# Performance work log

Measured on AMD Instinct MI355X. Metric: run time of the kernel, lower is better.

## Reference

```python
import jax, jax.numpy as jnp
import numpy as np

EMBED_DIM = 1024
NUM_HEADS = 16
HEAD_DIM = EMBED_DIM // NUM_HEADS
LN_EPS = 1e-5


def setup_inputs() -> dict:
    key = jax.random.key(0)
    ks = jax.random.split(key, 6)
    b, s, d = 2, 2048, EMBED_DIM
    scale = 1.0 / np.sqrt(d)
    x = jax.random.normal(ks[0], (b, s, d), dtype=jnp.float32)
    w_qkv = jax.random.normal(ks[1], (d, 3 * d), dtype=jnp.float32) * scale
    b_qkv = jax.random.normal(ks[2], (3 * d,), dtype=jnp.float32) * 0.02
    w_out = jax.random.normal(ks[3], (d, d), dtype=jnp.float32) * scale
    b_out = jax.random.normal(ks[4], (d,), dtype=jnp.float32) * 0.02
    gamma = jnp.ones((d,), dtype=jnp.float32)
    ln_beta = jnp.zeros((d,), dtype=jnp.float32)
    beta = jax.random.normal(ks[5], (), dtype=jnp.float32) * 0.1
    return {"x": x, "w_qkv": w_qkv, "b_qkv": b_qkv, "w_out": w_out,
            "b_out": b_out, "gamma": gamma, "ln_beta": ln_beta, "beta": beta}


def _layernorm(x, gamma, ln_beta):
    mu = jnp.mean(x, axis=-1, keepdims=True)
    var = jnp.mean(jnp.square(x - mu), axis=-1, keepdims=True)
    return (x - mu) * jax.lax.rsqrt(var + LN_EPS) * gamma + ln_beta


def reference(x, w_qkv, b_qkv, w_out, b_out, gamma, ln_beta, beta):
    b, s, d = x.shape
    h, hd = NUM_HEADS, HEAD_DIM
    residual = x
    xn = _layernorm(x, gamma, ln_beta)
    qkv = xn @ w_qkv + b_qkv                       # [b, s, 3d]
    qkv = qkv.reshape(b, s, 3, h, hd)
    q = jnp.transpose(qkv[:, :, 0], (0, 2, 1, 3))  # [b, h, s, hd]
    k = jnp.transpose(qkv[:, :, 1], (0, 2, 1, 3))
    v = jnp.transpose(qkv[:, :, 2], (0, 2, 1, 3))
    attn = jnp.einsum('bhqd,bhkd->bhqk', q, k) / np.sqrt(hd)
    idx = jnp.arange(s)
    dist = jnp.abs(idx[None, :] - idx[:, None]).astype(attn.dtype)  # [s, s]
    attn = attn + beta * jnp.log1p(dist)[None, None, :, :]
    probs = jax.nn.softmax(attn, axis=-1)
    ctx = jnp.einsum('bhqk,bhkd->bhqd', probs, v)  # [b, h, s, hd]
    ctx = jnp.transpose(ctx, (0, 2, 1, 3)).reshape(b, s, d)
    return residual + ctx @ w_out + b_out
```

## Files before the change

### kernel.cpp

```cpp
#include <hip/hip_runtime.h>

#define SEQ 2048
#define DIM 1024
#define NHEAD 16
#define HDIM 64
#define NTOK 4096
#define N3D 3072

typedef __attribute__((ext_vector_type(8))) short bf16x8;
typedef __attribute__((ext_vector_type(4))) float floatx4;
typedef __attribute__((ext_vector_type(4))) unsigned short ushortx4;

__device__ __forceinline__ unsigned short f2bf(float f) {
    unsigned int u = __builtin_bit_cast(unsigned int, f);
    u += 0x7FFFu + ((u >> 16) & 1u);
    return (unsigned short)(u >> 16);
}

__device__ __forceinline__ void async_copy16(const void* g, const void* l) {
    __builtin_amdgcn_global_load_lds(
        (const __attribute__((address_space(1))) unsigned int*)(unsigned long long)g,
        (__attribute__((address_space(3))) unsigned int*)(unsigned int)(unsigned long long)l,
        16, 0, 0);
}

#define MFMA_BF16(a, b, c) __builtin_amdgcn_mfma_f32_16x16x32_bf16((a), (b), (c), 0, 0, 0)

__global__ __launch_bounds__(256)
void transpose_cvt(const float* __restrict__ src, unsigned short* __restrict__ dst,
                   int rows, int cols) {
    __shared__ float tile[32][33];
    const int c0 = blockIdx.x * 32, r0 = blockIdx.y * 32;
    const int tx = threadIdx.x & 31, ty = threadIdx.x >> 5;
    for (int i = 0; i < 4; ++i) {
        int r = ty + i * 8;
        tile[r][tx] = src[(size_t)(r0 + r) * cols + c0 + tx];
    }
    __syncthreads();
    for (int i = 0; i < 4; ++i) {
        int rr = ty + i * 8;
        dst[(size_t)(c0 + rr) * rows + r0 + tx] = f2bf(tile[tx][rr]);
    }
}

__global__ __launch_bounds__(256)
void ln_kernel(const float* __restrict__ x, const float* __restrict__ gamma,
               const float* __restrict__ lnb, unsigned short* __restrict__ xn) {
    const int row = blockIdx.x;
    const int tid = threadIdx.x;
    const float* xr = x + (size_t)row * DIM;
    float4 v = ((const float4*)xr)[tid];
    float s = v.x + v.y + v.z + v.w;
    float s2 = v.x * v.x + v.y * v.y + v.z * v.z + v.w * v.w;
    for (int off = 1; off < 64; off <<= 1) {
        s += __shfl_xor(s, off, 64);
        s2 += __shfl_xor(s2, off, 64);
    }
    __shared__ float red[8];
    const int wave = tid >> 6, lane = tid & 63;
    if (lane == 0) { red[wave] = s; red[4 + wave] = s2; }
    __syncthreads();
    s = red[0] + red[1] + red[2] + red[3];
    s2 = red[4] + red[5] + red[6] + red[7];
    const float mu = s * (1.0f / DIM);
    const float var = s2 * (1.0f / DIM) - mu * mu;
    const float rstd = rsqrtf(var + 1e-5f);
    float4 g = ((const float4*)gamma)[tid];
    float4 bb = ((const float4*)lnb)[tid];
    unsigned short* o = xn + (size_t)row * DIM + tid * 4;
    o[0] = f2bf((v.x - mu) * rstd * g.x + bb.x);
    o[1] = f2bf((v.y - mu) * rstd * g.y + bb.y);
    o[2] = f2bf((v.z - mu) * rstd * g.z + bb.z);
    o[3] = f2bf((v.w - mu) * rstd * g.w + bb.w);
}

__global__ __launch_bounds__(256)
void qkv_gemm(const unsigned short* __restrict__ A, const unsigned short* __restrict__ Bt,
              const float* __restrict__ bias, unsigned short* __restrict__ qo,
              unsigned short* __restrict__ ko, unsigned short* __restrict__ vTo) {
    __shared__ unsigned short Asm[128 * 64];
    __shared__ unsigned short Bsm[128 * 64];
    const int tid = threadIdx.x;
    const int wave = tid >> 6, lane = tid & 63;
    const int quad = lane >> 4, r16 = lane & 15;
    const int m0 = blockIdx.y * 128, n0 = blockIdx.x * 128;
    const int wm = (wave & 1) * 64, wn = (wave >> 1) * 64;
    floatx4 acc[4][4] = {};
    for (int k0 = 0; k0 < DIM; k0 += 64) {
        __syncthreads();
        for (int p = 0; p < 4; ++p) {
            int s = tid + p * 256;
            int r = s >> 3, c8 = (s & 7) << 3;
            async_copy16(A + (size_t)(m0 + r) * DIM + k0 + c8, Asm + s * 8);
            async_copy16(Bt + (size_t)(n0 + r) * DIM + k0 + c8, Bsm + s * 8);
        }
        __syncthreads();
        for (int h = 0; h < 2; ++h) {
            bf16x8 af[4], bfr[4];
            for (int i = 0; i < 4; ++i)
                af[i] = *(const bf16x8*)(Asm + (wm + i * 16 + r16) * 64 + h * 32 + quad * 8);
            for (int j = 0; j < 4; ++j)
                bfr[j] = *(const bf16x8*)(Bsm + (wn + j * 16 + r16) * 64 + h * 32 + quad * 8);
            for (int i = 0; i < 4; ++i)
                for (int j = 0; j < 4; ++j)
                    acc[i][j] = MFMA_BF16(af[i], bfr[j], acc[i][j]);
        }
    }
    for (int j = 0; j < 4; ++j) {
        int n = n0 + wn + j * 16 + r16;
        float bn = bias[n];
        int part = n >> 10, nn = n & 1023;
        int head = nn >> 6, hdi = nn & 63;
        for (int i = 0; i < 4; ++i) {
            int mbase = m0 + wm + i * 16 + quad * 4;
            int bIdx = mbase >> 11, sIdx = mbase & 2047;
            if (part == 2) {
                ushortx4 pack;
                for (int e = 0; e < 4; ++e) pack[e] = f2bf(acc[i][j][e] + bn);
                *(ushortx4*)(vTo + ((size_t)(bIdx * NHEAD + head) * HDIM + hdi) * SEQ + sIdx) = pack;
            } else {
                unsigned short* dst = (part == 0) ? qo : ko;
                for (int e = 0; e < 4; ++e)
                    dst[((size_t)(bIdx * NHEAD + head) * SEQ + sIdx + e) * HDIM + hdi] =
                        f2bf(acc[i][j][e] + bn);
            }
        }
    }
}

__global__ __launch_bounds__(512)
void attn_kernel(const unsigned short* __restrict__ qg, const unsigned short* __restrict__ kg,
                 const unsigned short* __restrict__ vTg, const float* __restrict__ betap,
                 unsigned short* __restrict__ ctx) {
    __shared__ unsigned short QP[128][72];
    __shared__ unsigned short Kd[2][64 * 64];
    __shared__ unsigned short Vd[2][64 * 64];
    __shared__ float logt[SEQ];

    const int tid = threadIdx.x;
    const int wave = tid >> 6, lane = tid & 63;
    const int quad = lane >> 4, r16 = lane & 15;
    const int bh = blockIdx.y, qt = blockIdx.x;
    const int qBase = qt * 128;
    const float betaV = betap[0];
    const float L2E = 1.44269504f;
    const float c1 = 0.125f * L2E;

    for (int i = tid; i < SEQ; i += 512)
        logt[i] = betaV * log1pf((float)i) * L2E - 20.0f;

    const unsigned short* qptr = qg + ((size_t)bh * SEQ + qBase) * HDIM;
    for (int s = tid; s < 1024; s += 512) {
        int r = s >> 3, c8 = (s & 7) << 3;
        *(bf16x8*)(&QP[r][c8]) = *(const bf16x8*)(qptr + r * HDIM + c8);
    }

    const int sr = tid >> 3;
    const int scg = (tid & 7) ^ (sr & 7);
    const unsigned short* kbh = kg + (size_t)bh * SEQ * HDIM;
    const unsigned short* vbh = vTg + (size_t)bh * HDIM * SEQ;
    async_copy16(kbh + (size_t)sr * HDIM + scg * 8, &Kd[0][tid * 8]);
    async_copy16(vbh + (size_t)sr * SEQ + scg * 8, &Vd[0][tid * 8]);
    __syncthreads();

    bf16x8 qf0 = *(const bf16x8*)(&QP[wave * 16 + r16][quad * 8]);
    bf16x8 qf1 = *(const bf16x8*)(&QP[wave * 16 + r16][32 + quad * 8]);

    const bf16x8 onesv = {0x3F80, 0x3F80, 0x3F80, 0x3F80, 0x3F80, 0x3F80, 0x3F80, 0x3F80};

    floatx4 o[5] = {};
    const int qWaveBase = qBase + wave * 16;
    const int qrow0 = qWaveBase + quad * 4;

    for (int kt0 = 0; kt0 < SEQ; kt0 += 64) {
        const int buf = (kt0 >> 6) & 1;
        if (kt0 + 64 < SEQ) {
            async_copy16(kbh + (size_t)(kt0 + 64 + sr) * HDIM + scg * 8, &Kd[buf ^ 1][tid * 8]);
            async_copy16(vbh + (size_t)sr * SEQ + kt0 + 64 + scg * 8, &Vd[buf ^ 1][tid * 8]);
        }

        floatx4 sc[4];
        for (int ct = 0; ct < 4; ++ct) {
            int rK = ct * 16 + r16;
            const unsigned short* kb = &Kd[buf][rK * 64];
            bf16x8 kf0 = *(const bf16x8*)(kb + ((quad ^ (rK & 7)) << 3));
            bf16x8 kf1 = *(const bf16x8*)(kb + (((quad ^ 4) ^ (rK & 7)) << 3));
            floatx4 z = {0.f, 0.f, 0.f, 0.f};
            z = MFMA_BF16(qf0, kf0, z);
            z = MFMA_BF16(qf1, kf1, z);
            sc[ct] = z;
        }
        for (int ct = 0; ct < 4; ++ct) {
            const int keyTile = kt0 + ct * 16;
            const int key = keyTile + r16;
            if (qWaveBase >= keyTile + 16) {
                const float* lp = &logt[qrow0 - key];
                for (int i = 0; i < 4; ++i)
                    sc[ct][i] = __builtin_amdgcn_exp2f(sc[ct][i] * c1 + lp[i]);
            } else if (keyTile >= qWaveBase + 16) {
                const float* lp = &logt[key - qrow0 - 3];
                for (int i = 0; i < 4; ++i)
                    sc[ct][i] = __builtin_amdgcn_exp2f(sc[ct][i] * c1 + lp[3 - i]);
            } else {
                for (int i = 0; i < 4; ++i) {
                    int dist = qrow0 + i - key;
                    dist = dist < 0 ? -dist : dist;
                    sc[ct][i] = __builtin_amdgcn_exp2f(sc[ct][i] * c1 + logt[dist]);
                }
            }
        }
        for (int ct = 0; ct < 4; ++ct)
            for (int i = 0; i < 4; ++i)
                QP[wave * 16 + quad * 4 + i][ct * 16 + r16] = f2bf(sc[ct][i]);
        bf16x8 pf0 = *(const bf16x8*)(&QP[wave * 16 + r16][quad * 8]);
        bf16x8 pf1 = *(const bf16x8*)(&QP[wave * 16 + r16][32 + quad * 8]);
        for (int nt = 0; nt < 4; ++nt) {
            int rV = nt * 16 + r16;
            const unsigned short* vb = &Vd[buf][rV * 64];
            bf16x8 vf0 = *(const bf16x8*)(vb + ((quad ^ (rV & 7)) << 3));
            bf16x8 vf1 = *(const bf16x8*)(vb + (((quad ^ 4) ^ (rV & 7)) << 3));
            o[nt] = MFMA_BF16(pf0, vf0, o[nt]);
            o[nt] = MFMA_BF16(pf1, vf1, o[nt]);
        }
        o[4] = MFMA_BF16(pf0, onesv, o[4]);
        o[4] = MFMA_BF16(pf1, onesv, o[4]);

        __syncthreads();
    }

    const int b_ = bh >> 4, h_ = bh & 15;
    for (int i = 0; i < 4; ++i) {
        float inv = 1.0f / o[4][i];
        int qi = qBase + wave * 16 + quad * 4 + i;
        for (int nt = 0; nt < 4; ++nt) {
            int d = nt * 16 + r16;
            ctx[((size_t)(b_ * SEQ + qi)) * DIM + h_ * HDIM + d] = f2bf(o[nt][i] * inv);
        }
    }
}

__global__ __launch_bounds__(256)
void out_gemm(const unsigned short* __restrict__ A, const unsigned short* __restrict__ Bt,
              const float* __restrict__ bias, const float* __restrict__ resid,
              float* __restrict__ out) {
    __shared__ unsigned short Asm[128 * 64];
    __shared__ unsigned short Bsm[64 * 64];
    const int tid = threadIdx.x;
    const int wave = tid >> 6, lane = tid & 63;
    const int quad = lane >> 4, r16 = lane & 15;
    const int m0 = blockIdx.y * 128, n0 = blockIdx.x * 64;
    const int wm = (wave & 1) * 64, wn = (wave >> 1) * 32;
    floatx4 acc[4][2] = {};
    for (int k0 = 0; k0 < DIM; k0 += 64) {
        __syncthreads();
        for (int p = 0; p < 4; ++p) {
            int s = tid + p * 256;
            int r = s >> 3, c8 = (s & 7) << 3;
            async_copy16(A + (size_t)(m0 + r) * DIM + k0 + c8, Asm + s * 8);
        }
        for (int p = 0; p < 2; ++p) {
            int s = tid + p * 256;
            int r = s >> 3, c8 = (s & 7) << 3;
            async_copy16(Bt + (size_t)(n0 + r) * DIM + k0 + c8, Bsm + s * 8);
        }
        __syncthreads();
        for (int h = 0; h < 2; ++h) {
            bf16x8 af[4], bfr[2];
            for (int i = 0; i < 4; ++i)
                af[i] = *(const bf16x8*)(Asm + (wm + i * 16 + r16) * 64 + h * 32 + quad * 8);
            for (int j = 0; j < 2; ++j)
                bfr[j] = *(const bf16x8*)(Bsm + (wn + j * 16 + r16) * 64 + h * 32 + quad * 8);
            for (int i = 0; i < 4; ++i)
                for (int j = 0; j < 2; ++j)
                    acc[i][j] = MFMA_BF16(af[i], bfr[j], acc[i][j]);
        }
    }
    for (int i = 0; i < 4; ++i)
        for (int j = 0; j < 2; ++j)
            for (int e = 0; e < 4; ++e) {
                int m = m0 + wm + i * 16 + quad * 4 + e;
                int n = n0 + wn + j * 16 + r16;
                out[(size_t)m * DIM + n] = acc[i][j][e] + bias[n] + resid[(size_t)m * DIM + n];
            }
}

extern "C" void kernel_launch(void* const* d_in, const int* in_sizes, int n_in,
                              void* d_out, int out_size, void* d_ws, size_t ws_size,
                              hipStream_t stream) {
    const float* x     = (const float*)d_in[0];
    const float* w_qkv = (const float*)d_in[1];
    const float* b_qkv = (const float*)d_in[2];
    const float* w_out = (const float*)d_in[3];
    const float* b_out = (const float*)d_in[4];
    const float* gamma = (const float*)d_in[5];
    const float* ln_b  = (const float*)d_in[6];
    const float* beta  = (const float*)d_in[7];
    float* out = (float*)d_out;

    char* ws = (char*)d_ws;
    const size_t MB = 1u << 20;
    unsigned short* xn    = (unsigned short*)(ws);
    unsigned short* wqkvT = (unsigned short*)(ws + 8 * MB);
    unsigned short* woutT = (unsigned short*)(ws + 14 * MB);
    unsigned short* qb    = (unsigned short*)(ws + 16 * MB);
    unsigned short* kb    = (unsigned short*)(ws + 24 * MB);
    unsigned short* vTb   = (unsigned short*)(ws + 32 * MB);
    unsigned short* ctx   = xn;

    transpose_cvt<<<dim3(96, 32), 256, 0, stream>>>(w_qkv, wqkvT, DIM, N3D);
    transpose_cvt<<<dim3(32, 32), 256, 0, stream>>>(w_out, woutT, DIM, DIM);
    ln_kernel<<<NTOK, 256, 0, stream>>>(x, gamma, ln_b, xn);
    qkv_gemm<<<dim3(24, 32), 256, 0, stream>>>(xn, wqkvT, b_qkv, qb, kb, vTb);
    attn_kernel<<<dim3(SEQ / 128, 32), 512, 0, stream>>>(qb, kb, vTb, beta, ctx);
    out_gemm<<<dim3(16, 32), 256, 0, stream>>>(ctx, woutT, b_out, x, out);
}
```

Before: 233.1 us.

## Merge prep kernels, swizzle block order for XCDs, add MFMA setprio

The two weight-transpose launches and the layernorm launch become one prep kernel that dispatches on block index, which removes two kernel launches. The qkv GEMM, attention and output GEMM kernels remap their flat block index so that blocks sharing operands land on the same XCD (stride-8 swizzle), aiming for better L2 reuse. The attention kernel raises wave priority around its MFMA sections with s_setprio. The remapping assumes the grid size divides evenly by 8, and the priority hints may interact unpredictably with the wave scheduler.

After: 235.3 us. No clear change (+1.0%).

```diff
diff --git a/kernel.cpp b/kernel.cpp
--- a/kernel.cpp
+++ b/kernel.cpp
@@ -27,51 +27,55 @@
 #define MFMA_BF16(a, b, c) __builtin_amdgcn_mfma_f32_16x16x32_bf16((a), (b), (c), 0, 0, 0)
 
 __global__ __launch_bounds__(256)
-void transpose_cvt(const float* __restrict__ src, unsigned short* __restrict__ dst,
-                   int rows, int cols) {
-    __shared__ float tile[32][33];
-    const int c0 = blockIdx.x * 32, r0 = blockIdx.y * 32;
-    const int tx = threadIdx.x & 31, ty = threadIdx.x >> 5;
-    for (int i = 0; i < 4; ++i) {
-        int r = ty + i * 8;
-        tile[r][tx] = src[(size_t)(r0 + r) * cols + c0 + tx];
-    }
-    __syncthreads();
-    for (int i = 0; i < 4; ++i) {
-        int rr = ty + i * 8;
-        dst[(size_t)(c0 + rr) * rows + r0 + tx] = f2bf(tile[tx][rr]);
-    }
-}
-
-__global__ __launch_bounds__(256)
-void ln_kernel(const float* __restrict__ x, const float* __restrict__ gamma,
-               const float* __restrict__ lnb, unsigned short* __restrict__ xn) {
-    const int row = blockIdx.x;
+void prep_kernel(const float* __restrict__ w_qkv, unsigned short* __restrict__ wqkvT,
+                 const float* __restrict__ w_out, unsigned short* __restrict__ woutT,
+                 const float* __restrict__ x, const float* __restrict__ gamma,
+                 const float* __restrict__ lnb, unsigned short* __restrict__ xn) {
+    const int bid = blockIdx.x;
     const int tid = threadIdx.x;
-    const float* xr = x + (size_t)row * DIM;
-    float4 v = ((const float4*)xr)[tid];
-    float s = v.x + v.y + v.z + v.w;
-    float s2 = v.x * v.x + v.y * v.y + v.z * v.z + v.w * v.w;
-    for (int off = 1; off < 64; off <<= 1) {
-        s += __shfl_xor(s, off, 64);
-        s2 += __shfl_xor(s2, off, 64);
-    }
-    __shared__ float red[8];
-    const int wave = tid >> 6, lane = tid & 63;
-    if (lane == 0) { red[wave] = s; red[4 + wave] = s2; }
-    __syncthreads();
-    s = red[0] + red[1] + red[2] + red[3];
-    s2 = red[4] + red[5] + red[6] + red[7];
-    const float mu = s * (1.0f / DIM);
-    const float var = s2 * (1.0f / DIM) - mu * mu;
-    const float rstd = rsqrtf(var + 1e-5f);
-    float4 g = ((const float4*)gamma)[tid];
-    float4 bb = ((const float4*)lnb)[tid];
-    unsigned short* o = xn + (size_t)row * DIM + tid * 4;
-    o[0] = f2bf((v.x - mu) * rstd * g.x + bb.x);
-    o[1] = f2bf((v.y - mu) * rstd * g.y + bb.y);
-    o[2] = f2bf((v.z - mu) * rstd * g.z + bb.z);
-    o[3] = f2bf((v.w - mu) * rstd * g.w + bb.w);
+    if (bid < 4096) {
+        __shared__ float tile[32][33];
+        const float* src; unsigned short* dst; int cols, bx, by;
+        if (bid < 3072) { src = w_qkv; dst = wqkvT; cols = N3D; bx = bid % 96; by = bid / 96; }
+        else { int t = bid - 3072; src = w_out; dst = woutT; cols = DIM; bx = t & 31; by = t >> 5; }
+        const int c0 = bx * 32, r0 = by * 32;
+        const int tx = tid & 31, ty = tid >> 5;
+        for (int i = 0; i < 4; ++i) {
+            int r = ty + i * 8;
+            tile[r][tx] = src[(size_t)(r0 + r) * cols + c0 + tx];
+        }
+        __syncthreads();
+        for (int i = 0; i < 4; ++i) {
+            int rr = ty + i * 8;
+            dst[(size_t)(c0 + rr) * DIM + r0 + tx] = f2bf(tile[tx][rr]);
+        }
+    } else {
+        const int row = bid - 4096;
+        const float* xr = x + (size_t)row * DIM;
+        float4 v = ((const float4*)xr)[tid];
+        float s = v.x + v.y + v.z + v.w;
+        float s2 = v.x * v.x + v.y * v.y + v.z * v.z + v.w * v.w;
+        for (int off = 1; off < 64; off <<= 1) {
+            s += __shfl_xor(s, off, 64);
+            s2 += __shfl_xor(s2, off, 64);
+        }
+        __shared__ float red[8];
+        const int wave = tid >> 6, lane = tid & 63;
+        if (lane == 0) { red[wave] = s; red[4 + wave] = s2; }
+        __syncthreads();
+        s = red[0] + red[1] + red[2] + red[3];
+        s2 = red[4] + red[5] + red[6] + red[7];
+        const float mu = s * (1.0f / DIM);
+        const float var = s2 * (1.0f / DIM) - mu * mu;
+        const float rstd = rsqrtf(var + 1e-5f);
+        float4 g = ((const float4*)gamma)[tid];
+        float4 bb = ((const float4*)lnb)[tid];
+        unsigned short* o = xn + (size_t)row * DIM + tid * 4;
+        o[0] = f2bf((v.x - mu) * rstd * g.x + bb.x);
+        o[1] = f2bf((v.y - mu) * rstd * g.y + bb.y);
+        o[2] = f2bf((v.z - mu) * rstd * g.z + bb.z);
+        o[3] = f2bf((v.w - mu) * rstd * g.w + bb.w);
+    }
 }
 
 __global__ __launch_bounds__(256)
@@ -83,7 +87,9 @@
     const int tid = threadIdx.x;
     const int wave = tid >> 6, lane = tid & 63;
     const int quad = lane >> 4, r16 = lane & 15;
-    const int m0 = blockIdx.y * 128, n0 = blockIdx.x * 128;
+    const int flat = blockIdx.y * 24 + blockIdx.x;
+    const int swz = (flat & 7) * 96 + (flat >> 3);
+    const int m0 = (swz / 24) * 128, n0 = (swz % 24) * 128;
     const int wm = (wave & 1) * 64, wn = (wave >> 1) * 64;
     floatx4 acc[4][4] = {};
     for (int k0 = 0; k0 < DIM; k0 += 64) {
@@ -140,7 +146,9 @@
     const int tid = threadIdx.x;
     const int wave = tid >> 6, lane = tid & 63;
     const int quad = lane >> 4, r16 = lane & 15;
-    const int bh = blockIdx.y, qt = blockIdx.x;
+    const int flat = blockIdx.y * 16 + blockIdx.x;
+    const int swz = (flat & 7) * 64 + (flat >> 3);
+    const int bh = swz >> 4, qt = swz & 15;
     const int qBase = qt * 128;
     const float betaV = betap[0];
     const float L2E = 1.44269504f;
@@ -180,6 +188,7 @@
         }
 
         floatx4 sc[4];
+        __builtin_amdgcn_s_setprio(1);
         for (int ct = 0; ct < 4; ++ct) {
             int rK = ct * 16 + r16;
             const unsigned short* kb = &Kd[buf][rK * 64];
@@ -190,6 +199,7 @@
             z = MFMA_BF16(qf1, kf1, z);
             sc[ct] = z;
         }
+        __builtin_amdgcn_s_setprio(0);
         for (int ct = 0; ct < 4; ++ct) {
             const int keyTile = kt0 + ct * 16;
             const int key = keyTile + r16;
@@ -214,6 +224,7 @@
                 QP[wave * 16 + quad * 4 + i][ct * 16 + r16] = f2bf(sc[ct][i]);
         bf16x8 pf0 = *(const bf16x8*)(&QP[wave * 16 + r16][quad * 8]);
         bf16x8 pf1 = *(const bf16x8*)(&QP[wave * 16 + r16][32 + quad * 8]);
+        __builtin_amdgcn_s_setprio(1);
         for (int nt = 0; nt < 4; ++nt) {
             int rV = nt * 16 + r16;
             const unsigned short* vb = &Vd[buf][rV * 64];
@@ -224,6 +235,7 @@
         }
         o[4] = MFMA_BF16(pf0, onesv, o[4]);
         o[4] = MFMA_BF16(pf1, onesv, o[4]);
+        __builtin_amdgcn_s_setprio(0);
 
         __syncthreads();
     }
@@ -248,7 +260,9 @@
     const int tid = threadIdx.x;
     const int wave = tid >> 6, lane = tid & 63;
     const int quad = lane >> 4, r16 = lane & 15;
-    const int m0 = blockIdx.y * 128, n0 = blockIdx.x * 64;
+    const int flat = blockIdx.y * 16 + blockIdx.x;
+    const int swz = (flat & 7) * 64 + (flat >> 3);
+    const int m0 = (swz >> 4) * 128, n0 = (swz & 15) * 64;
     const int wm = (wave & 1) * 64, wn = (wave >> 1) * 32;
     floatx4 acc[4][2] = {};
     for (int k0 = 0; k0 < DIM; k0 += 64) {
@@ -307,9 +321,7 @@
     unsigned short* vTb   = (unsigned short*)(ws + 32 * MB);
     unsigned short* ctx   = xn;
 
-    transpose_cvt<<<dim3(96, 32), 256, 0, stream>>>(w_qkv, wqkvT, DIM, N3D);
-    transpose_cvt<<<dim3(32, 32), 256, 0, stream>>>(w_out, woutT, DIM, DIM);
-    ln_kernel<<<NTOK, 256, 0, stream>>>(x, gamma, ln_b, xn);
+    prep_kernel<<<8192, 256, 0, stream>>>(w_qkv, wqkvT, w_out, woutT, x, gamma, ln_b, xn);
     qkv_gemm<<<dim3(24, 32), 256, 0, stream>>>(xn, wqkvT, b_qkv, qb, kb, vTb);
     attn_kernel<<<dim3(SEQ / 128, 32), 512, 0, stream>>>(qb, kb, vTb, beta, ctx);
     out_gemm<<<dim3(16, 32), 256, 0, stream>>>(ctx, woutT, b_out, x, out);
```
